# Performance work log

Measured on AMD Instinct MI355X. Metric: run time of the kernel, lower is better.

The kernel has to match this reference:

```python
import jax, jax.numpy as jnp
import numpy as np

N_INST = 8  # max instance id; ids 1..N_INST, 0 = background
MESH_NORM = 1024.0  # from SegmantationLoss._meshgrid


def _meshgrid(H, W):
    y = jnp.arange(H, dtype=jnp.float32) / MESH_NORM
    x = jnp.arange(W, dtype=jnp.float32) / MESH_NORM
    return jnp.stack([jnp.broadcast_to(y[:, None], (H, W)),
                      jnp.broadcast_to(x[None, :], (H, W))], axis=0)  # [2,H,W]


def _lovasz_hinge_batch(logits, labels, delta=1.0):
    """logits, labels: [K,P] float. Returns [K] lovasz hinge losses."""
    signs = 2.0 * labels - 1.0
    errors = delta - logits * signs
    order = jnp.argsort(-errors, axis=1)  # descending
    es = jnp.take_along_axis(errors, order, axis=1)
    gs = jnp.take_along_axis(labels, order, axis=1)
    gts = gs.sum(axis=1, keepdims=True)
    intersection = gts - jnp.cumsum(gs, axis=1)
    union = gts + jnp.cumsum(1.0 - gs, axis=1)
    jac = 1.0 - intersection / union
    grad = jnp.concatenate([jac[:, :1], jac[:, 1:] - jac[:, :-1]], axis=1)
    return (jax.nn.relu(es) * grad).sum(axis=1)


def setup_inputs() -> dict:
    key = jax.random.key(0)
    k1, k2, k3, k4 = jax.random.split(key, 4)
    B, H, W = 4, 512, 1024
    x_vec = jax.random.normal(k1, (B, 2, H, W), dtype=jnp.float32)
    # small scale so psigma = exp(10*ppsigma) stays in a sane range
    x_sigma = jax.random.normal(k2, (B, 2, H, W), dtype=jnp.float32) * 0.03
    x_seed = jax.random.normal(k3, (B, 1, H, W), dtype=jnp.float32)
    t = jax.random.randint(k4, (B, H, W), 0, 9, dtype=jnp.int32)
    return {"x_vec": x_vec, "x_sigma": x_sigma, "x_seed": x_seed, "t": t}


def reference(x_vec, x_sigma, x_seed, t):
    B, _, H, W = x_vec.shape
    mesh = _meshgrid(H, W)

    emb = jnp.tanh(x_vec) + mesh[None]          # [B,2,H,W] spatial embedding
    ppsig = x_sigma                              # [B,2,H,W] pre-pseudo-sigma
    seed = jax.nn.sigmoid(x_seed)[:, 0]          # [B,H,W]

    ids = jnp.arange(1, N_INST + 1, dtype=t.dtype)
    mf = (t[None] == ids[:, None, None, None]).astype(jnp.float32)  # [N,B,H,W]
    cnt = mf.sum(axis=(2, 3))                    # [N,B]
    present = cnt > 0
    safe = jnp.maximum(cnt, 1.0)
    n_present = jnp.maximum(present.sum(axis=0).astype(jnp.float32), 1.0)  # [B]

    # per-instance masked means
    centroid = jnp.einsum('nbhw,bchw->nbc', mf, emb) / safe[..., None]    # [N,B,2]
    inst_pps = jnp.einsum('nbhw,bchw->nbc', mf, ppsig) / safe[..., None]  # [N,B,2]
    psigma = jnp.exp(10.0 * inst_pps)                                     # [N,B,2]

    # gaussian between pixel and instance embedding (l22n)
    diff2 = (emb[None] - centroid[..., None, None]) ** 2                  # [N,B,2,H,W]
    dist = (diff2 * psigma[..., None, None]).sum(axis=2)                  # [N,B,H,W]
    gauss = jnp.exp(-0.5 * dist)                                          # [N,B,H,W]

    # lovasz hinge per instance on logits 2*gauss - 1 over all pixels
    P = H * W
    lov = _lovasz_hinge_batch((2.0 * gauss - 1.0).reshape(N_INST * B, P),
                              mf.reshape(N_INST * B, P)).reshape(N_INST, B)
    lov = jnp.where(present, lov, 0.0)
    lovasz_loss = (lov.sum(axis=0) / n_present).mean()

    # sigma loss: pixel ppsigma -> detached instance mean ppsigma
    sd = (ppsig[None] - jax.lax.stop_gradient(inst_pps)[..., None, None]) ** 2
    sl = (sd.sum(axis=2) * mf).sum(axis=(2, 3)) / safe                    # [N,B]
    sl = jnp.where(present, sl, 0.0)
    sigma_loss = (sl.sum(axis=0) / n_present).mean()

    # seed loss: background -> 0, foreground -> detached gaussian
    bg = (t == 0).astype(jnp.float32)                                     # [B,H,W]
    bg_cnt = jnp.maximum(bg.sum(axis=(1, 2)), 1.0)
    bg_loss = ((seed ** 2) * bg).sum(axis=(1, 2)) / bg_cnt                # [B]
    fg = ((seed[None] - jax.lax.stop_gradient(gauss)) ** 2 * mf).sum(axis=(2, 3)) / safe
    fg = jnp.where(present, fg, 0.0)
    seed_loss = ((bg_loss + fg.sum(axis=0)) /
                 (1.0 + present.sum(axis=0).astype(jnp.float32))).mean()

    return lovasz_loss + sigma_loss + seed_loss
```

## Files before the change

### kernel.cpp

```cpp
#include <hip/hip_runtime.h>
#include <math.h>

#define B 4
#define H 512
#define W 1024
#define P (H*W)
#define NI 8
#define NSEG 32
#define NB 256
#define INV_BW ((float)NB/2.0f)
#define NSTRIP 256
#define STRIP_PX (P/NSTRIP)
#define K1B 512
#define K1PX (P/K1B)

#define D_CENY 0
#define D_CENX 32
#define D_PSY  64
#define D_PSX  96
#define D_CNT  128
#define D_SL   160
#define D_K4C  192
#define OFF_FGP 256
#define OFF_HIST (OFF_FGP + 9*1024)
#define OFF_FOLD (OFF_HIST + NSEG*NSTRIP*NB)
#define OFF_PK1  (OFF_FOLD + 8*NSEG*NB)

__device__ __forceinline__ float fast_tanh(float x) {
    float e = __expf(2.0f * x);
    return 1.0f - 2.0f / (e + 1.0f);
}
__device__ __forceinline__ float fast_sigmoid(float x) {
    return 1.0f / (1.0f + __expf(-x));
}
template<int CTRL, int RM>
__device__ __forceinline__ float dpp_add(float x) {
    int y = __builtin_amdgcn_update_dpp(0, __float_as_int(x), CTRL, RM, 0xF, true);
    return x + __int_as_float(y);
}
__device__ __forceinline__ float wred(float x) {
    x = dpp_add<0x111, 0xF>(x);
    x = dpp_add<0x112, 0xF>(x);
    x = dpp_add<0x114, 0xF>(x);
    x = dpp_add<0x118, 0xF>(x);
    x = dpp_add<0x142, 0xA>(x);
    x = dpp_add<0x143, 0xC>(x);
    return x;
}

__global__ __launch_bounds__(256) void k1_stats(const float* __restrict__ xv,
                                                const float* __restrict__ xs,
                                                const int*  __restrict__ t,
                                                float* __restrict__ pk1) {
    const int b = blockIdx.y, bx = blockIdx.x, tid = threadIdx.x;
    const int lane = tid & 63, wid = tid >> 6;
    const float* xv_y = xv + (size_t)b*2*P;
    const float* xv_x = xv_y + P;
    const float* xs_y = xs + (size_t)b*2*P;
    const float* xs_x = xs_y + P;
    const int*   tb   = t + (size_t)b*P;

    float cnt[NI], sey[NI], sex[NI], sgy[NI], sgx[NI], sq[NI];
    #pragma unroll
    for (int n = 0; n < NI; ++n) { cnt[n]=0.f; sey[n]=0.f; sex[n]=0.f; sgy[n]=0.f; sgx[n]=0.f; sq[n]=0.f; }

    int p0 = bx*K1PX + tid*4;
    float4 vy = *(const float4*)(xv_y + p0);
    float4 vx = *(const float4*)(xv_x + p0);
    float4 sy = *(const float4*)(xs_y + p0);
    float4 sx = *(const float4*)(xs_x + p0);
    int4   tt = *(const int4*)(tb + p0);
    #pragma unroll
    for (int j = 0; j < 4; ++j) {
        int pix = p0 + j;
        float ey = fast_tanh((&vy.x)[j]) + (float)(pix >> 10) * (1.0f/1024.0f);
        float ex = fast_tanh((&vx.x)[j]) + (float)(pix & 1023) * (1.0f/1024.0f);
        float gy = (&sy.x)[j], gx = (&sx.x)[j];
        int tv = (&tt.x)[j];
        float q = gy*gy + gx*gx;
        #pragma unroll
        for (int n = 0; n < NI; ++n) {
            float m = (tv == n+1) ? 1.0f : 0.0f;
            cnt[n] += m; sey[n] += m*ey; sex[n] += m*ex;
            sgy[n] += m*gy; sgx[n] += m*gx; sq[n] += m*q;
        }
    }
    __shared__ float sw[4*64];
    #define RED48(val, slot) { float r_ = wred(val); if (lane == 63) sw[wid*64 + (slot)] = r_; }
    #pragma unroll
    for (int n = 0; n < NI; ++n) {
        RED48(cnt[n], n*6+0); RED48(sey[n], n*6+1); RED48(sex[n], n*6+2);
        RED48(sgy[n], n*6+3); RED48(sgx[n], n*6+4); RED48(sq[n],  n*6+5);
    }
    #undef RED48
    __syncthreads();
    if (tid < 48) {
        float s = sw[tid] + sw[64+tid] + sw[128+tid] + sw[192+tid];
        pk1[(size_t)(b*K1B + bx)*64 + tid] = s;
    }
}

__global__ __launch_bounds__(1024) void k2_finalize(float* __restrict__ wsf,
                                                    const float* __restrict__ pk1,
                                                    float* __restrict__ out) {
    const int tid = threadIdx.x;
    __shared__ float part[16*64];
    __shared__ float ssum[4*64];
    const int v = tid & 63, g = tid >> 6;
    const int b = g >> 2, c = g & 3;
    float acc = 0.f;
    const int jbase = b*K1B + c*128;
    #pragma unroll 8
    for (int i = 0; i < 128; ++i) acc += pk1[(size_t)(jbase + i)*64 + v];
    part[g*64 + v] = acc;
    __syncthreads();
    if (tid < 256) {
        int vb = tid & 63, bb = tid >> 6;
        ssum[bb*64+vb] = part[(bb*4+0)*64+vb] + part[(bb*4+1)*64+vb]
                       + part[(bb*4+2)*64+vb] + part[(bb*4+3)*64+vb];
    }
    __syncthreads();
    if (tid < NSEG) {
        int n = tid >> 2, bb = tid & 3;
        float cv  = ssum[bb*64 + n*6+0];
        float sey = ssum[bb*64 + n*6+1];
        float sex = ssum[bb*64 + n*6+2];
        float sgy = ssum[bb*64 + n*6+3];
        float sgx = ssum[bb*64 + n*6+4];
        float sq  = ssum[bb*64 + n*6+5];
        float safe = fmaxf(cv, 1.0f);
        float ipy = sgy/safe, ipx = sgx/safe;
        wsf[D_CENY+tid] = sey/safe;
        wsf[D_CENX+tid] = sex/safe;
        wsf[D_PSY+tid]  = expf(10.0f*ipy);
        wsf[D_PSX+tid]  = expf(10.0f*ipx);
        wsf[D_CNT+tid]  = cv;
        wsf[D_SL+tid]   = sq/safe - (ipy*ipy + ipx*ipx);
    } else if (tid < 64) {
        ((unsigned*)wsf)[D_K4C + (tid - 32)] = 0u;
    } else if (tid == 64) {
        out[0] = 0.f;
    }
}

__global__ __launch_bounds__(512) void k3_hist(const float* __restrict__ xv,
                                               const float* __restrict__ xseed,
                                               const int*  __restrict__ t,
                                               const float* __restrict__ wsf,
                                               unsigned* __restrict__ hist_g,
                                               float* __restrict__ fgp) {
    const int strip = blockIdx.x;
    const int b     = blockIdx.y;
    const int tid   = threadIdx.x;
    const int lane  = tid & 63;

    __shared__ unsigned hist[NI*NB];
    *((uint4*)hist + tid) = (uint4){0u,0u,0u,0u};
    __shared__ float spar[4*NI];
    if (tid < 4*NI) {
        int n = tid & (NI-1), q = tid >> 3;
        spar[tid] = wsf[q*32 + n*B + b];
    }
    __syncthreads();

    float ceny[NI], cenx[NI], psy[NI], psx[NI], fgn[NI];
    #pragma unroll
    for (int n = 0; n < NI; ++n) {
        ceny[n] = spar[n]; cenx[n] = spar[NI+n];
        psy[n] = spar[2*NI+n]; psx[n] = spar[3*NI+n];
        fgn[n] = 0.f;
    }
    float bgq = 0.f;

    const float* xv_y = xv + (size_t)b*2*P;
    const float* xv_x = xv_y + P;
    const float* sdp  = xseed + (size_t)b*P;
    const int*   tb   = t + (size_t)b*P;

    {
        int p0 = strip * STRIP_PX + tid*4;
        float4 vy = *(const float4*)(xv_y + p0);
        float4 vx = *(const float4*)(xv_x + p0);
        float4 se = *(const float4*)(sdp + p0);
        int4   tt = *(const int4*)(tb + p0);
        #pragma unroll
        for (int j = 0; j < 4; ++j) {
            int pix = p0 + j;
            float ey = fast_tanh((&vy.x)[j]) + (float)(pix >> 10) * (1.0f/1024.0f);
            float ex = fast_tanh((&vx.x)[j]) + (float)(pix & 1023) * (1.0f/1024.0f);
            int tv = (&tt.x)[j];
            float gown = 0.f;
            #pragma unroll
            for (int n = 0; n < NI; ++n) {
                float dy = ey - ceny[n], dx = ex - cenx[n];
                float g = __expf(-0.5f * (psy[n]*dy*dy + psx[n]*dx*dx));
                bool lab = (tv == n+1);
                float err = lab ? (2.0f - 2.0f*g) : (2.0f*g);
                int key = (int)(err * INV_BW);
                key = key > (NB-1) ? (NB-1) : key;
                if (key > 0) atomicAdd(&hist[n*NB + key], lab ? 0x10000u : 1u);
                if (lab) gown = g;
            }
            float s = fast_sigmoid((&se.x)[j]);
            if (tv > 0) {
                float d = s - gown;
                float dd = d*d;
                #pragma unroll
                for (int n = 0; n < NI; ++n) fgn[n] += (tv == n+1) ? dd : 0.f;
            } else {
                bgq += s*s;
            }
        }
    }
    __syncthreads();
    {
        int lin = tid*4;
        int n = lin >> 8, key = lin & (NB-1);
        uint4 v = *(const uint4*)&hist[lin];
        *(uint4*)&hist_g[((size_t)((n*4 + b)*NSTRIP + strip))*NB + key] = v;
    }
    __shared__ float sfg[NI+1];
    if (tid < NI+1) sfg[tid] = 0.f;
    __syncthreads();
    #pragma unroll
    for (int n = 0; n < NI; ++n) {
        float r = wred(fgn[n]);
        if (lane == 63 && r != 0.f) atomicAdd(&sfg[n], r);
    }
    {
        float r = wred(bgq);
        if (lane == 63) atomicAdd(&sfg[NI], r);
    }
    __syncthreads();
    if (tid < NI+1) fgp[tid*1024 + b*NSTRIP + strip] = sfg[tid];
}

__global__ __launch_bounds__(256) void k4_fused(const unsigned* __restrict__ hist_g,
                                                unsigned* __restrict__ fold,
                                                float* __restrict__ wsf,
                                                const float* __restrict__ fgp,
                                                float* __restrict__ out) {
    const int q = blockIdx.x;
    const int seg = blockIdx.y;
    const int tid = threadIdx.x;

    unsigned posk, negk;
    {
        const unsigned* src = hist_g + (size_t)(seg*NSTRIP + q*64)*NB + tid;
        unsigned pos = 0u, neg = 0u;
        #pragma unroll 8
        for (int s = 0; s < 64; ++s) {
            unsigned v = src[(size_t)s*NB];
            pos += v >> 16; neg += v & 0xffffu;
        }
        fold[((size_t)q*NSEG + seg)*NB + tid] = pos;
        fold[(size_t)4*NSEG*NB + ((size_t)q*NSEG + seg)*NB + tid] = neg;
        posk = pos; negk = neg;
    }

    __shared__ unsigned slast;
    __syncthreads();
    if (tid == 0) {
        __threadfence();
        unsigned* cnt4 = (unsigned*)wsf + D_K4C;
        slast = __hip_atomic_fetch_add(&cnt4[seg], 1u, __ATOMIC_ACQ_REL,
                                       __HIP_MEMORY_SCOPE_AGENT);
    }
    __syncthreads();
    if (slast != 3u) return;
    __threadfence();

    const int n = seg >> 2, b = seg & 3;
    __shared__ float scnt[NSEG];
    __shared__ float sfr[256];
    __shared__ unsigned up[256], un[256];
    __shared__ double sdd[256];
    if (tid < NSEG) scnt[tid] = wsf[D_CNT + tid];
    __syncthreads();

    if (n == 0) {
        sfr[tid] = fgp[NI*1024 + b*NSTRIP + tid];
        __syncthreads();
        #pragma unroll
        for (int d = 128; d > 0; d >>= 1) {
            if (tid < d) sfr[tid] += sfr[tid + d];
            __syncthreads();
        }
        if (tid == 0) {
            float bgs = sfr[0];
            int np = 0; float ss = 0.f, csum = 0.f;
            for (int k = 0; k < NI; ++k) {
                float cv = scnt[k*4 + b];
                csum += cv;
                if (cv > 0.5f) { np++; ss += wsf[D_SL + k*4 + b]; }
            }
            float bgc = fmaxf((float)P - csum, 1.0f);
            float bgl = bgs / bgc;
            float npf = fmaxf((float)np, 1.0f);
            atomicAdd(out, (ss/npf + bgl/(1.0f + (float)np)) * (1.0f/(float)B));
        }
        __syncthreads();
    }

    const float G = scnt[seg];
    if (G < 0.5f) return;
    int npc = 0;
    #pragma unroll
    for (int k = 0; k < NI; ++k) npc += (scnt[k*4 + b] > 0.5f) ? 1 : 0;

    sfr[tid] = fgp[n*1024 + b*NSTRIP + tid];
    __syncthreads();
    #pragma unroll
    for (int d = 128; d > 0; d >>= 1) {
        if (tid < d) sfr[tid] += sfr[tid + d];
        __syncthreads();
    }
    const float FG = sfr[0];

    unsigned pos = posk, neg = negk;
    #pragma unroll
    for (int qq = 0; qq < 4; ++qq) {
        if (qq == q) continue;
        pos += fold[((size_t)qq*NSEG + seg)*NB + tid];
        neg += fold[(size_t)4*NSEG*NB + ((size_t)qq*NSEG + seg)*NB + tid];
    }

    up[tid] = pos; un[tid] = neg;
    __syncthreads();
    for (int d = 1; d < 256; d <<= 1) {
        unsigned ap = (tid + d < 256) ? up[tid + d] : 0u;
        unsigned an = (tid + d < 256) ? un[tid + d] : 0u;
        __syncthreads();
        up[tid] += ap; un[tid] += an;
        __syncthreads();
    }
    const unsigned TP = up[0], TN = un[0];
    const unsigned Gu = (unsigned)(G + 0.5f);
    const unsigned NEGu = (unsigned)P - Gu;
    unsigned cump = up[tid] - pos;
    unsigned cumn = un[tid] - neg;

    const double dG = (double)G;
    double acc = 0.0;
    {
        unsigned cp = pos, cn = neg;
        if (tid == 0) { cp = Gu - TP; cn = NEGu - TN; }
        if (cp | cn) {
            unsigned ep = cump, en = cumn;
            unsigned epi = ep + cp, eni = en + cn;
            double jb = 1.0 - (dG - (double)ep)  / (dG + (double)en);
            double ja = 1.0 - (dG - (double)epi) / (dG + (double)eni);
            acc = (((double)tid + 0.5) * (2.0/(double)NB)) * (ja - jb);
        }
    }
    sdd[tid] = acc;
    __syncthreads();
    #pragma unroll
    for (int d = 128; d > 0; d >>= 1) {
        if (tid < d) sdd[tid] += sdd[tid + d];
        __syncthreads();
    }
    if (tid == 0) {
        float npf = fmaxf((float)npc, 1.0f);
        float val = (float)sdd[0] / (npf * (float)B)
                  + (FG / G) / ((1.0f + (float)npc) * (float)B);
        atomicAdd(out, val);
    }
}

extern "C" void kernel_launch(void* const* d_in, const int* in_sizes, int n_in,
                              void* d_out, int out_size, void* d_ws, size_t ws_size,
                              hipStream_t stream) {
    (void)in_sizes; (void)n_in; (void)out_size; (void)ws_size;
    const float* xv  = (const float*)d_in[0];
    const float* xs  = (const float*)d_in[1];
    const float* xsd = (const float*)d_in[2];
    const int*   t   = (const int*)d_in[3];
    float* wsf = (float*)d_ws;
    unsigned* hist_g = (unsigned*)d_ws + OFF_HIST;
    unsigned* fold   = (unsigned*)d_ws + OFF_FOLD;
    float* pk1 = wsf + OFF_PK1;
    float* fgp = wsf + OFF_FGP;
    float* out = (float*)d_out;

    k1_stats<<<dim3(K1B, B), 256, 0, stream>>>(xv, xs, t, pk1);
    k2_finalize<<<1, 1024, 0, stream>>>(wsf, pk1, out);
    k3_hist<<<dim3(NSTRIP, B), 512, 0, stream>>>(xv, xsd, t, wsf, hist_g, fgp);
    k4_fused<<<dim3(4, NSEG), 256, 0, stream>>>(hist_g, fold, wsf, fgp, out);
}
```

Baseline: 132.6 us.

## Prescale gaussian parameters to cut per-pixel math, and process more pixels per stats block

The finalize kernel now stores sqrt(psigma*0.5*log2e) and prescaled centroids, so the histogram kernel computes the gaussian with two FMAs, one FMA-square and a single exp2 that yields the histogram key (256*g) directly. This replaces the subtract, multiply and scale sequence in the hot 8-instance loop. Separately, the stats kernel handles four float4 chunks per thread with a quarter as many blocks, which shrinks the partial-sum buffer and the finalize reduction. The algebraic rewrite may shift rounding near bin boundaries slightly.

```diff
diff --git a/kernel.cpp b/kernel.cpp
--- a/kernel.cpp
+++ b/kernel.cpp
@@ -8,16 +8,15 @@
 #define NI 8
 #define NSEG 32
 #define NB 256
-#define INV_BW ((float)NB/2.0f)
 #define NSTRIP 256
 #define STRIP_PX (P/NSTRIP)
-#define K1B 512
+#define K1B 128
 #define K1PX (P/K1B)
 
-#define D_CENY 0
-#define D_CENX 32
-#define D_PSY  64
-#define D_PSX  96
+#define D_CYP  0
+#define D_CXP  32
+#define D_AY   64
+#define D_AX   96
 #define D_CNT  128
 #define D_SL   160
 #define D_K4C  192
@@ -64,25 +63,28 @@
     #pragma unroll
     for (int n = 0; n < NI; ++n) { cnt[n]=0.f; sey[n]=0.f; sex[n]=0.f; sgy[n]=0.f; sgx[n]=0.f; sq[n]=0.f; }
 
-    int p0 = bx*K1PX + tid*4;
-    float4 vy = *(const float4*)(xv_y + p0);
-    float4 vx = *(const float4*)(xv_x + p0);
-    float4 sy = *(const float4*)(xs_y + p0);
-    float4 sx = *(const float4*)(xs_x + p0);
-    int4   tt = *(const int4*)(tb + p0);
-    #pragma unroll
-    for (int j = 0; j < 4; ++j) {
-        int pix = p0 + j;
-        float ey = fast_tanh((&vy.x)[j]) + (float)(pix >> 10) * (1.0f/1024.0f);
-        float ex = fast_tanh((&vx.x)[j]) + (float)(pix & 1023) * (1.0f/1024.0f);
-        float gy = (&sy.x)[j], gx = (&sx.x)[j];
-        int tv = (&tt.x)[j];
-        float q = gy*gy + gx*gx;
+    #pragma unroll
+    for (int it = 0; it < 4; ++it) {
+        int p0 = bx*K1PX + it*1024 + tid*4;
+        float4 vy = *(const float4*)(xv_y + p0);
+        float4 vx = *(const float4*)(xv_x + p0);
+        float4 sy = *(const float4*)(xs_y + p0);
+        float4 sx = *(const float4*)(xs_x + p0);
+        int4   tt = *(const int4*)(tb + p0);
         #pragma unroll
-        for (int n = 0; n < NI; ++n) {
-            float m = (tv == n+1) ? 1.0f : 0.0f;
-            cnt[n] += m; sey[n] += m*ey; sex[n] += m*ex;
-            sgy[n] += m*gy; sgx[n] += m*gx; sq[n] += m*q;
+        for (int j = 0; j < 4; ++j) {
+            int pix = p0 + j;
+            float ey = fast_tanh((&vy.x)[j]) + (float)(pix >> 10) * (1.0f/1024.0f);
+            float ex = fast_tanh((&vx.x)[j]) + (float)(pix & 1023) * (1.0f/1024.0f);
+            float gy = (&sy.x)[j], gx = (&sx.x)[j];
+            int tv = (&tt.x)[j];
+            float q = gy*gy + gx*gx;
+            #pragma unroll
+            for (int n = 0; n < NI; ++n) {
+                float m = (tv == n+1) ? 1.0f : 0.0f;
+                cnt[n] += m; sey[n] += m*ey; sex[n] += m*ex;
+                sgy[n] += m*gy; sgx[n] += m*gx; sq[n] += m*q;
+            }
         }
     }
     __shared__ float sw[4*64];
@@ -109,9 +111,9 @@
     const int v = tid & 63, g = tid >> 6;
     const int b = g >> 2, c = g & 3;
     float acc = 0.f;
-    const int jbase = b*K1B + c*128;
+    const int jbase = b*K1B + c*32;
     #pragma unroll 8
-    for (int i = 0; i < 128; ++i) acc += pk1[(size_t)(jbase + i)*64 + v];
+    for (int i = 0; i < 32; ++i) acc += pk1[(size_t)(jbase + i)*64 + v];
     part[g*64 + v] = acc;
     __syncthreads();
     if (tid < 256) {
@@ -130,12 +132,16 @@
         float sq  = ssum[bb*64 + n*6+5];
         float safe = fmaxf(cv, 1.0f);
         float ipy = sgy/safe, ipx = sgx/safe;
-        wsf[D_CENY+tid] = sey/safe;
-        wsf[D_CENX+tid] = sex/safe;
-        wsf[D_PSY+tid]  = expf(10.0f*ipy);
-        wsf[D_PSX+tid]  = expf(10.0f*ipx);
-        wsf[D_CNT+tid]  = cv;
-        wsf[D_SL+tid]   = sq/safe - (ipy*ipy + ipx*ipx);
+        float ceny = sey/safe, cenx = sex/safe;
+        const float hl2e = 0.7213475204444817f;
+        float ay = sqrtf(expf(10.0f*ipy) * hl2e);
+        float ax = sqrtf(expf(10.0f*ipx) * hl2e);
+        wsf[D_AY+tid]  = ay;
+        wsf[D_AX+tid]  = ax;
+        wsf[D_CYP+tid] = ay*ceny;
+        wsf[D_CXP+tid] = ax*cenx;
+        wsf[D_CNT+tid] = cv;
+        wsf[D_SL+tid]  = sq/safe - (ipy*ipy + ipx*ipx);
     } else if (tid < 64) {
         ((unsigned*)wsf)[D_K4C + (tid - 32)] = 0u;
     } else if (tid == 64) {
@@ -163,11 +169,11 @@
     }
     __syncthreads();
 
-    float ceny[NI], cenx[NI], psy[NI], psx[NI], fgn[NI];
+    float cyp[NI], cxp[NI], ay[NI], ax[NI], fgn[NI];
     #pragma unroll
     for (int n = 0; n < NI; ++n) {
-        ceny[n] = spar[n]; cenx[n] = spar[NI+n];
-        psy[n] = spar[2*NI+n]; psx[n] = spar[3*NI+n];
+        cyp[n] = spar[n]; cxp[n] = spar[NI+n];
+        ay[n] = spar[2*NI+n]; ax[n] = spar[3*NI+n];
         fgn[n] = 0.f;
     }
     float bgq = 0.f;
@@ -192,14 +198,16 @@
             float gown = 0.f;
             #pragma unroll
             for (int n = 0; n < NI; ++n) {
-                float dy = ey - ceny[n], dx = ex - cenx[n];
-                float g = __expf(-0.5f * (psy[n]*dy*dy + psx[n]*dx*dx));
+                float dyp = fmaf(ey, ay[n], -cyp[n]);
+                float dxp = fmaf(ex, ax[n], -cxp[n]);
+                float e = fmaf(dxp, dxp, dyp*dyp);
+                float kg = exp2f(8.0f - e);
                 bool lab = (tv == n+1);
-                float err = lab ? (2.0f - 2.0f*g) : (2.0f*g);
-                int key = (int)(err * INV_BW);
+                float sel = lab ? (256.0f - kg) : kg;
+                int key = (int)sel;
                 key = key > (NB-1) ? (NB-1) : key;
                 if (key > 0) atomicAdd(&hist[n*NB + key], lab ? 0x10000u : 1u);
-                if (lab) gown = g;
+                if (lab) gown = kg * 0.00390625f;
             }
             float s = fast_sigmoid((&se.x)[j]);
             if (tv > 0) {
```

Result: faster. 128.6 us (-3.0%).
